# Kernel tuning notes

Measured on AMD Instinct MI355X. Metric: run time of the kernel, lower is better.

Reference implementation:

```python
import jax, jax.numpy as jnp
import numpy as np

NUM_EXPERTS = 8
TOP_K = 2
HIDDEN = 2048
INTER = 2816  # 2*INTER = 5632 fused gate+up
NUM_TOKENS = 8192


def setup_inputs() -> dict:
    key = jax.random.key(0)
    k1, k2, k3, k4 = jax.random.split(key, 4)
    hidden_states = jax.random.normal(k1, (NUM_TOKENS, HIDDEN), dtype=jnp.float32)
    gate_w = jax.random.normal(k2, (NUM_EXPERTS, HIDDEN), dtype=jnp.float32) * 0.02
    w13 = jax.random.normal(k3, (NUM_EXPERTS, 2 * INTER, HIDDEN), dtype=jnp.float32) * 0.02
    w2 = jax.random.normal(k4, (NUM_EXPERTS, HIDDEN, INTER), dtype=jnp.float32) * 0.02
    return {"hidden_states": hidden_states, "gate_w": gate_w, "w13": w13, "w2": w2}


def reference(hidden_states, gate_w, w13, w2):
    x = hidden_states  # [T, H]
    # Gate: ReplicatedLinear (no bias) -> router logits [T, E]
    router_logits = jnp.einsum('th,eh->te', x, gate_w)
    probs = jax.nn.softmax(router_logits, axis=-1)
    # top-k routing, renormalize=False: use softmax probs directly
    topk_vals, topk_idx = jax.lax.top_k(probs, TOP_K)  # [T, K]
    # combine weights [T, E]: sum of one-hot(topk_idx) * topk_vals
    cw = jnp.sum(jax.nn.one_hot(topk_idx, NUM_EXPERTS, dtype=x.dtype) * topk_vals[..., None], axis=1)
    # Dense per-expert grouped GEMM, masked combine (E is small and fixed)
    out = jnp.zeros_like(x)
    for e in range(NUM_EXPERTS):
        gu = jnp.einsum('th,ih->ti', x, w13[e])          # [T, 2I]
        g, u = gu[:, :INTER], gu[:, INTER:]
        h = jax.nn.silu(g) * u                            # SiLU-gated
        y = jnp.einsum('ti,hi->th', h, w2[e])             # [T, H]
        out = out + cw[:, e:e + 1] * y
    return out
```

## Files before the change

kernel.cpp:

```cpp
#include <hip/hip_runtime.h>
#include <stdint.h>
#include <stddef.h>

#define NE 8
#define HIDDEN 2048
#define INTER 2816
#define NT 8192
#define NROWS (NT * 2)

typedef __bf16 bf16x8 __attribute__((ext_vector_type(8)));
typedef float f32x4 __attribute__((ext_vector_type(4)));

__device__ __forceinline__ unsigned short f2bf(float f) {
  union { float f; uint32_t u; } v; v.f = f;
  uint32_t r = v.u + 0x7FFFu + ((v.u >> 16) & 1u);
  return (unsigned short)(r >> 16);
}

__device__ __forceinline__ void async16(const void* g, const unsigned short* lds_ptr) {
  __builtin_amdgcn_global_load_lds(
      (const __attribute__((address_space(1))) uint32_t*)g,
      (__attribute__((address_space(3))) uint32_t*)lds_ptr,
      16, 0, 0);
}

__global__ void cvt_kernel(const float4* __restrict__ src, ushort4* __restrict__ dst) {
  size_t i = (size_t)blockIdx.x * blockDim.x + threadIdx.x;
  float4 v = src[i];
  ushort4 o;
  o.x = f2bf(v.x); o.y = f2bf(v.y); o.z = f2bf(v.z); o.w = f2bf(v.w);
  dst[i] = o;
}

__global__ __launch_bounds__(256) void router_kernel(
    const float* __restrict__ x, const float* __restrict__ gw,
    int* __restrict__ top_e, float* __restrict__ top_w, int* __restrict__ counts) {
  int t = blockIdx.x * 4 + (threadIdx.x >> 6);
  int lane = threadIdx.x & 63;
  const float* xr = x + (size_t)t * HIDDEN;
  float acc[NE];
#pragma unroll
  for (int e = 0; e < NE; ++e) acc[e] = 0.f;
  for (int kb = 0; kb < HIDDEN; kb += 64) {
    float xv = xr[kb + lane];
#pragma unroll
    for (int e = 0; e < NE; ++e) acc[e] += xv * gw[e * HIDDEN + kb + lane];
  }
#pragma unroll
  for (int e = 0; e < NE; ++e) {
#pragma unroll
    for (int off = 32; off > 0; off >>= 1) acc[e] += __shfl_xor(acc[e], off, 64);
  }
  if (lane == 0) {
    float mx = acc[0];
#pragma unroll
    for (int e = 1; e < NE; ++e) mx = fmaxf(mx, acc[e]);
    float p[NE];
    float s = 0.f;
#pragma unroll
    for (int e = 0; e < NE; ++e) { p[e] = expf(acc[e] - mx); s += p[e]; }
    int e1 = 0;
#pragma unroll
    for (int e = 1; e < NE; ++e) if (p[e] > p[e1]) e1 = e;
    int e2 = (e1 == 0) ? 1 : 0;
#pragma unroll
    for (int e = 0; e < NE; ++e) if (e != e1 && p[e] > p[e2]) e2 = e;
    float inv = 1.f / s;
    top_e[2 * t] = e1; top_e[2 * t + 1] = e2;
    top_w[2 * t] = p[e1] * inv; top_w[2 * t + 1] = p[e2] * inv;
    atomicAdd(&counts[e1], 1);
    atomicAdd(&counts[e2], 1);
  }
}

__global__ void scan_kernel(const int* __restrict__ counts, int* __restrict__ offs) {
  if (threadIdx.x == 0) {
    int s = 0;
    for (int e = 0; e < NE; ++e) { offs[e] = s; s += counts[e]; }
    offs[NE] = s;
  }
}

__global__ void fill_kernel(const int* __restrict__ top_e, const float* __restrict__ top_w,
                            const int* __restrict__ offs, int* __restrict__ fillc,
                            int* __restrict__ row_tok, float* __restrict__ row_w,
                            int* __restrict__ row_of) {
  int t = blockIdx.x * 256 + threadIdx.x;
#pragma unroll
  for (int j = 0; j < 2; ++j) {
    int e = top_e[2 * t + j];
    int slot = atomicAdd(&fillc[e], 1);
    int row = offs[e] + slot;
    row_tok[row] = t;
    row_w[row] = top_w[2 * t + j];
    row_of[2 * t + j] = row;
  }
}

__global__ __launch_bounds__(512, 2) void gemm1_kernel(
    const unsigned short* __restrict__ xb, const unsigned short* __restrict__ w13b,
    const int* __restrict__ row_tok, const int* __restrict__ offs,
    unsigned short* __restrict__ hbuf) {
  __shared__ __align__(16) unsigned short smem[4][16384];
  const int e = blockIdx.z, mt = blockIdx.y, nt = blockIdx.x;
  const int row0 = offs[e];
  const int cnt = offs[e + 1] - row0;
  if (mt * 256 >= cnt) return;
  const int tid = threadIdx.x;

  const int lrow = tid >> 2;
  const int gch = ((tid & 3) ^ ((lrow >> 1) & 3)) * 8;
  size_t aA[2];
#pragma unroll
  for (int i = 0; i < 2; ++i) {
    int grow = mt * 256 + i * 128 + lrow;
    int rr = row0 + (grow < cnt ? grow : cnt - 1);
    aA[i] = (size_t)row_tok[rr] * HIDDEN + gch;
  }
  const size_t aBg = ((size_t)e * 2 * INTER + nt * 128 + lrow) * (size_t)HIDDEN + gch;
  const size_t aBu = ((size_t)e * 2 * INTER + INTER + nt * 128 + lrow) * (size_t)HIDDEN + gch;

  const int wv = tid >> 6, wm = wv >> 1, wn = wv & 1;
  const int l = tid & 63, lm = l & 15, lq = l >> 4;
  const int loff = lm * 32 + ((lq ^ ((lm >> 1) & 3)) * 8);

  f32x4 accg[4][4], accu[4][4];
#pragma unroll
  for (int i = 0; i < 4; ++i)
#pragma unroll
    for (int j = 0; j < 4; ++j) {
      accg[i][j] = (f32x4){0.f, 0.f, 0.f, 0.f};
      accu[i][j] = (f32x4){0.f, 0.f, 0.f, 0.f};
    }

#define ST_A1(P) do { \
    size_t ko = (size_t)(P) * 32; unsigned short* sD = &smem[(P) & 3][0]; \
    async16(xb + aA[0] + ko, sD + tid * 8); \
    async16(xb + aA[1] + ko, sD + 4096 + tid * 8); } while (0)
#define ST_B1(P) do { \
    size_t ko = (size_t)(P) * 32; unsigned short* sD = &smem[(P) & 3][0]; \
    async16(w13b + aBg + ko, sD + 8192 + tid * 8); \
    async16(w13b + aBu + ko, sD + 12288 + tid * 8); } while (0)

  const int NP = HIDDEN / 32;
  ST_A1(0); ST_B1(0); ST_A1(1); ST_B1(1); ST_A1(2); ST_B1(2);
  asm volatile("s_waitcnt vmcnt(8)" ::: "memory");
  __builtin_amdgcn_s_barrier();

  for (int p = 0; p < NP; ++p) {
    const unsigned short* sK = &smem[p & 3][0];
    const bool pf = (p + 3 < NP);
    bf16x8 af[4], bfr[4];
#pragma unroll
    for (int i = 0; i < 4; ++i)
      af[i] = *(const bf16x8*)(sK + (wm * 64 + i * 16) * 32 + loff);
#pragma unroll
    for (int j = 0; j < 4; ++j)
      bfr[j] = *(const bf16x8*)(sK + (256 + wn * 64 + j * 16) * 32 + loff);
    if (pf) ST_A1(p + 3);
    __builtin_amdgcn_s_barrier();
    asm volatile("s_waitcnt lgkmcnt(0)" ::: "memory");
    __builtin_amdgcn_sched_barrier(0);
    __builtin_amdgcn_s_setprio(1);
#pragma unroll
    for (int i = 0; i < 4; ++i)
#pragma unroll
      for (int j = 0; j < 4; ++j)
        accg[i][j] = __builtin_amdgcn_mfma_f32_16x16x32_bf16(af[i], bfr[j], accg[i][j], 0, 0, 0);
    __builtin_amdgcn_s_setprio(0);
    __builtin_amdgcn_s_barrier();
#pragma unroll
    for (int j = 0; j < 4; ++j)
      bfr[j] = *(const bf16x8*)(sK + (384 + wn * 64 + j * 16) * 32 + loff);
    if (pf) ST_B1(p + 3);
    if (pf)                  { asm volatile("s_waitcnt vmcnt(8)" ::: "memory"); }
    else if (p + 2 < NP)     { asm volatile("s_waitcnt vmcnt(4)" ::: "memory"); }
    else                     { asm volatile("s_waitcnt vmcnt(0)" ::: "memory"); }
    __builtin_amdgcn_s_barrier();
    asm volatile("s_waitcnt lgkmcnt(0)" ::: "memory");
    __builtin_amdgcn_sched_barrier(0);
    __builtin_amdgcn_s_setprio(1);
#pragma unroll
    for (int i = 0; i < 4; ++i)
#pragma unroll
      for (int j = 0; j < 4; ++j)
        accu[i][j] = __builtin_amdgcn_mfma_f32_16x16x32_bf16(af[i], bfr[j], accu[i][j], 0, 0, 0);
    __builtin_amdgcn_s_setprio(0);
    __builtin_amdgcn_s_barrier();
  }
#undef ST_A1
#undef ST_B1

#pragma unroll
  for (int i = 0; i < 4; ++i) {
#pragma unroll
    for (int r = 0; r < 4; ++r) {
      int grow = mt * 256 + wm * 64 + i * 16 + lq * 4 + r;
      if (grow < cnt) {
        size_t hrow = (size_t)(row0 + grow) * INTER + nt * 128 + wn * 64 + lm;
#pragma unroll
        for (int j = 0; j < 4; ++j) {
          float g = accg[i][j][r], u = accu[i][j][r];
          float sg = g / (1.f + expf(-g));
          hbuf[hrow + j * 16] = f2bf(sg * u);
        }
      }
    }
  }
}

__global__ __launch_bounds__(512, 2) void gemm2_kernel(
    const unsigned short* __restrict__ hbuf, const unsigned short* __restrict__ w2b,
    const float* __restrict__ row_w, const int* __restrict__ offs,
    float* __restrict__ ybuf) {
  __shared__ __align__(16) unsigned short smem[4][16384];
  const int e = blockIdx.z, mt = blockIdx.y, nt = blockIdx.x;
  const int row0 = offs[e];
  const int cnt = offs[e + 1] - row0;
  if (mt * 256 >= cnt) return;
  const int tid = threadIdx.x;

  const int lrow = tid >> 2;
  const int gch = ((tid & 3) ^ ((lrow >> 1) & 3)) * 8;
  size_t aA[2], aB[2];
#pragma unroll
  for (int i = 0; i < 2; ++i) {
    int grow = mt * 256 + i * 128 + lrow;
    int rr = row0 + (grow < cnt ? grow : cnt - 1);
    aA[i] = (size_t)rr * INTER + gch;
    aB[i] = ((size_t)e * HIDDEN + nt * 256 + i * 128 + lrow) * (size_t)INTER + gch;
  }

  const int wv = tid >> 6, wm = wv >> 1, wn = wv & 1;
  const int l = tid & 63, lm = l & 15, lq = l >> 4;
  const int loff = lm * 32 + ((lq ^ ((lm >> 1) & 3)) * 8);

  f32x4 acc[4][8];
#pragma unroll
  for (int i = 0; i < 4; ++i)
#pragma unroll
    for (int j = 0; j < 8; ++j) acc[i][j] = (f32x4){0.f, 0.f, 0.f, 0.f};

#define ST_A2(P) do { \
    size_t ko = (size_t)(P) * 32; unsigned short* sD = &smem[(P) & 3][0]; \
    async16(hbuf + aA[0] + ko, sD + tid * 8); \
    async16(hbuf + aA[1] + ko, sD + 4096 + tid * 8); } while (0)
#define ST_B2(P) do { \
    size_t ko = (size_t)(P) * 32; unsigned short* sD = &smem[(P) & 3][0]; \
    async16(w2b + aB[0] + ko, sD + 8192 + tid * 8); \
    async16(w2b + aB[1] + ko, sD + 12288 + tid * 8); } while (0)

  const int NP = INTER / 32;
  ST_A2(0); ST_B2(0); ST_A2(1); ST_B2(1); ST_A2(2); ST_B2(2);
  asm volatile("s_waitcnt vmcnt(8)" ::: "memory");
  __builtin_amdgcn_s_barrier();

  for (int p = 0; p < NP; ++p) {
    const unsigned short* sK = &smem[p & 3][0];
    const bool pf = (p + 3 < NP);
    bf16x8 af[4], bfr[4];
#pragma unroll
    for (int i = 0; i < 4; ++i)
      af[i] = *(const bf16x8*)(sK + (wm * 64 + i * 16) * 32 + loff);
#pragma unroll
    for (int j = 0; j < 4; ++j)
      bfr[j] = *(const bf16x8*)(sK + (256 + wn * 128 + j * 16) * 32 + loff);
    if (pf) ST_A2(p + 3);
    __builtin_amdgcn_s_barrier();
    asm volatile("s_waitcnt lgkmcnt(0)" ::: "memory");
    __builtin_amdgcn_sched_barrier(0);
    __builtin_amdgcn_s_setprio(1);
#pragma unroll
    for (int i = 0; i < 4; ++i)
#pragma unroll
      for (int j = 0; j < 4; ++j)
        acc[i][j] = __builtin_amdgcn_mfma_f32_16x16x32_bf16(af[i], bfr[j], acc[i][j], 0, 0, 0);
    __builtin_amdgcn_s_setprio(0);
    __builtin_amdgcn_s_barrier();
#pragma unroll
    for (int j = 0; j < 4; ++j)
      bfr[j] = *(const bf16x8*)(sK + (256 + wn * 128 + (j + 4) * 16) * 32 + loff);
    if (pf) ST_B2(p + 3);
    if (pf)                  { asm volatile("s_waitcnt vmcnt(8)" ::: "memory"); }
    else if (p + 2 < NP)     { asm volatile("s_waitcnt vmcnt(4)" ::: "memory"); }
    else                     { asm volatile("s_waitcnt vmcnt(0)" ::: "memory"); }
    __builtin_amdgcn_s_barrier();
    asm volatile("s_waitcnt lgkmcnt(0)" ::: "memory");
    __builtin_amdgcn_sched_barrier(0);
    __builtin_amdgcn_s_setprio(1);
#pragma unroll
    for (int i = 0; i < 4; ++i)
#pragma unroll
      for (int j = 0; j < 4; ++j)
        acc[i][j + 4] = __builtin_amdgcn_mfma_f32_16x16x32_bf16(af[i], bfr[j], acc[i][j + 4], 0, 0, 0);
    __builtin_amdgcn_s_setprio(0);
    __builtin_amdgcn_s_barrier();
  }
#undef ST_A2
#undef ST_B2

#pragma unroll
  for (int i = 0; i < 4; ++i) {
#pragma unroll
    for (int r = 0; r < 4; ++r) {
      int grow = mt * 256 + wm * 64 + i * 16 + lq * 4 + r;
      if (grow < cnt) {
        int rr = row0 + grow;
        float w = row_w[rr];
        float* yrow = ybuf + (size_t)rr * HIDDEN + nt * 256 + wn * 128 + lm;
#pragma unroll
        for (int j = 0; j < 8; ++j) yrow[j * 16] = w * acc[i][j][r];
      }
    }
  }
}

__global__ __launch_bounds__(256) void combine_kernel(
    const float* __restrict__ ybuf, const int* __restrict__ row_of,
    float* __restrict__ out) {
  int t = blockIdx.x;
  int r0 = row_of[2 * t], r1 = row_of[2 * t + 1];
  const float4* y0 = (const float4*)(ybuf + (size_t)r0 * HIDDEN);
  const float4* y1 = (const float4*)(ybuf + (size_t)r1 * HIDDEN);
  float4* o = (float4*)(out + (size_t)t * HIDDEN);
#pragma unroll
  for (int it = 0; it < 2; ++it) {
    int c = it * 256 + threadIdx.x;
    float4 a = y0[c], b = y1[c];
    o[c] = make_float4(a.x + b.x, a.y + b.y, a.z + b.z, a.w + b.w);
  }
}

extern "C" void kernel_launch(void* const* d_in, const int* in_sizes, int n_in,
                              void* d_out, int out_size, void* d_ws, size_t ws_size,
                              hipStream_t stream) {
  const float* x = (const float*)d_in[0];
  const float* gw = (const float*)d_in[1];
  const float* w13 = (const float*)d_in[2];
  const float* w2 = (const float*)d_in[3];
  float* out = (float*)d_out;
  char* ws = (char*)d_ws;

  int* counts = (int*)(ws + 0);
  int* fillc = (int*)(ws + 32);
  int* offs = (int*)(ws + 64);
  int* top_e = (int*)(ws + 1024);
  float* top_w = (float*)(ws + 66560);
  int* row_tok = (int*)(ws + 132096);
  float* row_w = (float*)(ws + 197632);
  int* row_of = (int*)(ws + 263168);
  unsigned short* xb = (unsigned short*)(ws + 328704);
  unsigned short* w13b = (unsigned short*)(ws + 33883136);
  float* ybuf = (float*)(ws + 33883136);
  unsigned short* w2b = (unsigned short*)(ws + 218432512);
  unsigned short* hb = (unsigned short*)(ws + 310707200);

  hipMemsetAsync(ws, 0, 1024, stream);

  cvt_kernel<<<16384, 256, 0, stream>>>((const float4*)x, (ushort4*)xb);
  cvt_kernel<<<90112, 256, 0, stream>>>((const float4*)w13, (ushort4*)w13b);
  cvt_kernel<<<45056, 256, 0, stream>>>((const float4*)w2, (ushort4*)w2b);

  router_kernel<<<2048, 256, 0, stream>>>(x, gw, top_e, top_w, counts);
  scan_kernel<<<1, 64, 0, stream>>>(counts, offs);
  fill_kernel<<<32, 256, 0, stream>>>(top_e, top_w, offs, fillc, row_tok, row_w, row_of);

  gemm1_kernel<<<dim3(22, 32, 8), 512, 0, stream>>>(xb, w13b, row_tok, offs, hb);
  gemm2_kernel<<<dim3(8, 32, 8), 512, 0, stream>>>(hb, w2b, row_w, offs, ybuf);
  combine_kernel<<<8192, 256, 0, stream>>>(ybuf, row_of, out);
}
```

Baseline: 1.675 ms.

## Unroll K loops by four and use one barrier per k-step

Both grouped-GEMM main loops are unrolled by four, so the four LDS ring slots become compile-time constants. Each k-step now ends with a single barrier instead of four. In the gate/up GEMM, the gate and up B fragments are loaded together and their MFMAs are interleaved, and all prefetches for a step are issued at once. The aim is to cut barrier stalls and give the scheduler longer uninterrupted MFMA streams. The cost is extra VGPRs for the second B fragment set, which could reduce occupancy.

```diff
diff --git a/kernel.cpp b/kernel.cpp
--- a/kernel.cpp
+++ b/kernel.cpp
@@ -133,61 +133,50 @@
       accu[i][j] = (f32x4){0.f, 0.f, 0.f, 0.f};
     }
 
-#define ST_A1(P) do { \
-    size_t ko = (size_t)(P) * 32; unsigned short* sD = &smem[(P) & 3][0]; \
+  const int NP = HIDDEN / 32;
+
+#define ST_A1(SL, P) do { \
+    size_t ko = (size_t)(P) * 32; unsigned short* sD = &smem[(SL)][0]; \
     async16(xb + aA[0] + ko, sD + tid * 8); \
     async16(xb + aA[1] + ko, sD + 4096 + tid * 8); } while (0)
-#define ST_B1(P) do { \
-    size_t ko = (size_t)(P) * 32; unsigned short* sD = &smem[(P) & 3][0]; \
+#define ST_B1(SL, P) do { \
+    size_t ko = (size_t)(P) * 32; unsigned short* sD = &smem[(SL)][0]; \
     async16(w13b + aBg + ko, sD + 8192 + tid * 8); \
     async16(w13b + aBu + ko, sD + 12288 + tid * 8); } while (0)
 
-  const int NP = HIDDEN / 32;
-  ST_A1(0); ST_B1(0); ST_A1(1); ST_B1(1); ST_A1(2); ST_B1(2);
+#define PAIR1(C) do { \
+    const unsigned short* sK = &smem[(C)][0]; \
+    const int p_ = pb + (C); \
+    bf16x8 af[4], bg[4], bu[4]; \
+    _Pragma("unroll") for (int i = 0; i < 4; ++i) \
+      af[i] = *(const bf16x8*)(sK + (wm * 64 + i * 16) * 32 + loff); \
+    _Pragma("unroll") for (int j = 0; j < 4; ++j) \
+      bg[j] = *(const bf16x8*)(sK + (256 + wn * 64 + j * 16) * 32 + loff); \
+    _Pragma("unroll") for (int j = 0; j < 4; ++j) \
+      bu[j] = *(const bf16x8*)(sK + (384 + wn * 64 + j * 16) * 32 + loff); \
+    if (p_ + 3 < NP) { ST_A1(((C) + 3) & 3, p_ + 3); ST_B1(((C) + 3) & 3, p_ + 3); } \
+    __builtin_amdgcn_s_setprio(1); \
+    _Pragma("unroll") for (int i = 0; i < 4; ++i) \
+      _Pragma("unroll") for (int j = 0; j < 4; ++j) { \
+        accg[i][j] = __builtin_amdgcn_mfma_f32_16x16x32_bf16(af[i], bg[j], accg[i][j], 0, 0, 0); \
+        accu[i][j] = __builtin_amdgcn_mfma_f32_16x16x32_bf16(af[i], bu[j], accu[i][j], 0, 0, 0); \
+      } \
+    __builtin_amdgcn_s_setprio(0); \
+    asm volatile("s_waitcnt lgkmcnt(0)" ::: "memory"); \
+    if (p_ + 3 < NP)      { asm volatile("s_waitcnt vmcnt(8)" ::: "memory"); } \
+    else if (p_ + 2 < NP) { asm volatile("s_waitcnt vmcnt(4)" ::: "memory"); } \
+    else                  { asm volatile("s_waitcnt vmcnt(0)" ::: "memory"); } \
+    __builtin_amdgcn_s_barrier(); \
+  } while (0)
+
+  ST_A1(0, 0); ST_B1(0, 0); ST_A1(1, 1); ST_B1(1, 1); ST_A1(2, 2); ST_B1(2, 2);
   asm volatile("s_waitcnt vmcnt(8)" ::: "memory");
   __builtin_amdgcn_s_barrier();
 
-  for (int p = 0; p < NP; ++p) {
-    const unsigned short* sK = &smem[p & 3][0];
-    const bool pf = (p + 3 < NP);
-    bf16x8 af[4], bfr[4];
-#pragma unroll
-    for (int i = 0; i < 4; ++i)
-      af[i] = *(const bf16x8*)(sK + (wm * 64 + i * 16) * 32 + loff);
-#pragma unroll
-    for (int j = 0; j < 4; ++j)
-      bfr[j] = *(const bf16x8*)(sK + (256 + wn * 64 + j * 16) * 32 + loff);
-    if (pf) ST_A1(p + 3);
-    __builtin_amdgcn_s_barrier();
-    asm volatile("s_waitcnt lgkmcnt(0)" ::: "memory");
-    __builtin_amdgcn_sched_barrier(0);
-    __builtin_amdgcn_s_setprio(1);
-#pragma unroll
-    for (int i = 0; i < 4; ++i)
-#pragma unroll
-      for (int j = 0; j < 4; ++j)
-        accg[i][j] = __builtin_amdgcn_mfma_f32_16x16x32_bf16(af[i], bfr[j], accg[i][j], 0, 0, 0);
-    __builtin_amdgcn_s_setprio(0);
-    __builtin_amdgcn_s_barrier();
-#pragma unroll
-    for (int j = 0; j < 4; ++j)
-      bfr[j] = *(const bf16x8*)(sK + (384 + wn * 64 + j * 16) * 32 + loff);
-    if (pf) ST_B1(p + 3);
-    if (pf)                  { asm volatile("s_waitcnt vmcnt(8)" ::: "memory"); }
-    else if (p + 2 < NP)     { asm volatile("s_waitcnt vmcnt(4)" ::: "memory"); }
-    else                     { asm volatile("s_waitcnt vmcnt(0)" ::: "memory"); }
-    __builtin_amdgcn_s_barrier();
-    asm volatile("s_waitcnt lgkmcnt(0)" ::: "memory");
-    __builtin_amdgcn_sched_barrier(0);
-    __builtin_amdgcn_s_setprio(1);
-#pragma unroll
-    for (int i = 0; i < 4; ++i)
-#pragma unroll
-      for (int j = 0; j < 4; ++j)
-        accu[i][j] = __builtin_amdgcn_mfma_f32_16x16x32_bf16(af[i], bfr[j], accu[i][j], 0, 0, 0);
-    __builtin_amdgcn_s_setprio(0);
-    __builtin_amdgcn_s_barrier();
-  }
+  for (int pb = 0; pb < NP; pb += 4) {
+    PAIR1(0); PAIR1(1); PAIR1(2); PAIR1(3);
+  }
+#undef PAIR1
 #undef ST_A1
 #undef ST_B1
 
@@ -241,61 +230,53 @@
 #pragma unroll
     for (int j = 0; j < 8; ++j) acc[i][j] = (f32x4){0.f, 0.f, 0.f, 0.f};
 
-#define ST_A2(P) do { \
-    size_t ko = (size_t)(P) * 32; unsigned short* sD = &smem[(P) & 3][0]; \
+  const int NP = INTER / 32;
+
+#define ST_A2(SL, P) do { \
+    size_t ko = (size_t)(P) * 32; unsigned short* sD = &smem[(SL)][0]; \
     async16(hbuf + aA[0] + ko, sD + tid * 8); \
     async16(hbuf + aA[1] + ko, sD + 4096 + tid * 8); } while (0)
-#define ST_B2(P) do { \
-    size_t ko = (size_t)(P) * 32; unsigned short* sD = &smem[(P) & 3][0]; \
+#define ST_B2(SL, P) do { \
+    size_t ko = (size_t)(P) * 32; unsigned short* sD = &smem[(SL)][0]; \
     async16(w2b + aB[0] + ko, sD + 8192 + tid * 8); \
     async16(w2b + aB[1] + ko, sD + 12288 + tid * 8); } while (0)
 
-  const int NP = INTER / 32;
-  ST_A2(0); ST_B2(0); ST_A2(1); ST_B2(1); ST_A2(2); ST_B2(2);
+#define PAIR2(C) do { \
+    const unsigned short* sK = &smem[(C)][0]; \
+    const int p_ = pb + (C); \
+    bf16x8 af[4], b0[4], b1[4]; \
+    _Pragma("unroll") for (int i = 0; i < 4; ++i) \
+      af[i] = *(const bf16x8*)(sK + (wm * 64 + i * 16) * 32 + loff); \
+    _Pragma("unroll") for (int j = 0; j < 4; ++j) \
+      b0[j] = *(const bf16x8*)(sK + (256 + wn * 128 + j * 16) * 32 + loff); \
+    if (p_ + 3 < NP) { ST_A2(((C) + 3) & 3, p_ + 3); ST_B2(((C) + 3) & 3, p_ + 3); } \
+    __builtin_amdgcn_s_setprio(1); \
+    _Pragma("unroll") for (int i = 0; i < 4; ++i) \
+      _Pragma("unroll") for (int j = 0; j < 4; ++j) \
+        acc[i][j] = __builtin_amdgcn_mfma_f32_16x16x32_bf16(af[i], b0[j], acc[i][j], 0, 0, 0); \
+    __builtin_amdgcn_s_setprio(0); \
+    _Pragma("unroll") for (int j = 0; j < 4; ++j) \
+      b1[j] = *(const bf16x8*)(sK + (256 + wn * 128 + (j + 4) * 16) * 32 + loff); \
+    __builtin_amdgcn_s_setprio(1); \
+    _Pragma("unroll") for (int i = 0; i < 4; ++i) \
+      _Pragma("unroll") for (int j = 0; j < 4; ++j) \
+        acc[i][j + 4] = __builtin_amdgcn_mfma_f32_16x16x32_bf16(af[i], b1[j], acc[i][j + 4], 0, 0, 0); \
+    __builtin_amdgcn_s_setprio(0); \
+    asm volatile("s_waitcnt lgkmcnt(0)" ::: "memory"); \
+    if (p_ + 3 < NP)      { asm volatile("s_waitcnt vmcnt(8)" ::: "memory"); } \
+    else if (p_ + 2 < NP) { asm volatile("s_waitcnt vmcnt(4)" ::: "memory"); } \
+    else                  { asm volatile("s_waitcnt vmcnt(0)" ::: "memory"); } \
+    __builtin_amdgcn_s_barrier(); \
+  } while (0)
+
+  ST_A2(0, 0); ST_B2(0, 0); ST_A2(1, 1); ST_B2(1, 1); ST_A2(2, 2); ST_B2(2, 2);
   asm volatile("s_waitcnt vmcnt(8)" ::: "memory");
   __builtin_amdgcn_s_barrier();
 
-  for (int p = 0; p < NP; ++p) {
-    const unsigned short* sK = &smem[p & 3][0];
-    const bool pf = (p + 3 < NP);
-    bf16x8 af[4], bfr[4];
-#pragma unroll
-    for (int i = 0; i < 4; ++i)
-      af[i] = *(const bf16x8*)(sK + (wm * 64 + i * 16) * 32 + loff);
-#pragma unroll
-    for (int j = 0; j < 4; ++j)
-      bfr[j] = *(const bf16x8*)(sK + (256 + wn * 128 + j * 16) * 32 + loff);
-    if (pf) ST_A2(p + 3);
-    __builtin_amdgcn_s_barrier();
-    asm volatile("s_waitcnt lgkmcnt(0)" ::: "memory");
-    __builtin_amdgcn_sched_barrier(0);
-    __builtin_amdgcn_s_setprio(1);
-#pragma unroll
-    for (int i = 0; i < 4; ++i)
-#pragma unroll
-      for (int j = 0; j < 4; ++j)
-        acc[i][j] = __builtin_amdgcn_mfma_f32_16x16x32_bf16(af[i], bfr[j], acc[i][j], 0, 0, 0);
-    __builtin_amdgcn_s_setprio(0);
-    __builtin_amdgcn_s_barrier();
-#pragma unroll
-    for (int j = 0; j < 4; ++j)
-      bfr[j] = *(const bf16x8*)(sK + (256 + wn * 128 + (j + 4) * 16) * 32 + loff);
-    if (pf) ST_B2(p + 3);
-    if (pf)                  { asm volatile("s_waitcnt vmcnt(8)" ::: "memory"); }
-    else if (p + 2 < NP)     { asm volatile("s_waitcnt vmcnt(4)" ::: "memory"); }
-    else                     { asm volatile("s_waitcnt vmcnt(0)" ::: "memory"); }
-    __builtin_amdgcn_s_barrier();
-    asm volatile("s_waitcnt lgkmcnt(0)" ::: "memory");
-    __builtin_amdgcn_sched_barrier(0);
-    __builtin_amdgcn_s_setprio(1);
-#pragma unroll
-    for (int i = 0; i < 4; ++i)
-#pragma unroll
-      for (int j = 0; j < 4; ++j)
-        acc[i][j + 4] = __builtin_amdgcn_mfma_f32_16x16x32_bf16(af[i], bfr[j], acc[i][j + 4], 0, 0, 0);
-    __builtin_amdgcn_s_setprio(0);
-    __builtin_amdgcn_s_barrier();
-  }
+  for (int pb = 0; pb < NP; pb += 4) {
+    PAIR2(0); PAIR2(1); PAIR2(2); PAIR2(3);
+  }
+#undef PAIR2
 #undef ST_A2
 #undef ST_B2
 
```

Result: slower. 2.068 ms (+23.4%).
